# Kernel tuning notes

Hardware: AMD Instinct MI355X
Metric: run time of the kernel (lower is better)

The kernel has to match this reference:

```python
import jax, jax.numpy as jnp
import numpy as np

L, H, P = 16384, 512, 512
DT_MIN, DT_MAX = 1e-3, 1e-1


def setup_inputs() -> dict:
    key = jax.random.key(0)
    ks = jax.random.split(key, 9)
    u = jax.random.normal(ks[0], (L, H), dtype=jnp.float32)
    # stable diagonal state matrix: Re(Lambda) < 0 (HiPPO-style init)
    Lambda_re = -(0.5 * jax.random.uniform(ks[1], (P,), dtype=jnp.float32) + 1e-3)
    Lambda_im = jnp.pi * jax.random.normal(ks[2], (P,), dtype=jnp.float32)
    # lecun-normal-ish scaling for B (fan-in H) and C (fan-in P)
    B_re = jax.random.normal(ks[3], (P, H), dtype=jnp.float32) / jnp.sqrt(2.0 * H)
    B_im = jax.random.normal(ks[4], (P, H), dtype=jnp.float32) / jnp.sqrt(2.0 * H)
    C_re = jax.random.normal(ks[5], (H, P), dtype=jnp.float32) / jnp.sqrt(2.0 * P)
    C_im = jax.random.normal(ks[6], (H, P), dtype=jnp.float32) / jnp.sqrt(2.0 * P)
    D = jax.random.uniform(ks[7], (H,), dtype=jnp.float32)
    # init_log_steps: uniform in [log(dt_min), log(dt_max)]
    lo, hi = np.log(DT_MIN), np.log(DT_MAX)
    log_step = jax.random.uniform(ks[8], (P,), dtype=jnp.float32, minval=lo, maxval=hi)
    return {"u": u, "Lambda_re": Lambda_re, "Lambda_im": Lambda_im,
            "B_re": B_re, "B_im": B_im, "C_re": C_re, "C_im": C_im,
            "D": D, "log_step": log_step}


def _binary_op(q_i, q_j):
    # associative combine for diagonal linear recurrence (elementwise over (L, P))
    A_i, b_i = q_i
    A_j, b_j = q_j
    return (A_j * A_i, A_j * b_i + b_j)


def reference(u, Lambda_re, Lambda_im, B_re, B_im, C_re, C_im, D, log_step):
    Lambda = Lambda_re + 1j * Lambda_im            # (P,) complex64
    B_tilde = B_re + 1j * B_im                     # (P, H)
    C_tilde = C_re + 1j * C_im                     # (H, P)
    step = jnp.exp(log_step)                       # (P,)
    # zero-order-hold discretization
    Lambda_bar = jnp.exp(Lambda * step)            # (P,)
    B_bar = ((Lambda_bar - 1.0) / Lambda)[:, None] * B_tilde  # (P, H)
    # Bu_t = B_bar @ u_t for all t, as one GEMM: (L, H) @ (H, P)
    Bu = u.astype(B_bar.dtype) @ B_bar.T           # (L, P) complex
    Lambda_el = jnp.broadcast_to(Lambda_bar, Bu.shape)  # (L, P)
    _, xs = jax.lax.associative_scan(_binary_op, (Lambda_el, Bu))  # xs: (L, P)
    # y_t = Re(C_tilde @ x_t) + D * u_t, batched as one GEMM
    ys = (xs @ C_tilde.T).real + D * u             # (L, H)
    return ys.astype(jnp.float32)
```

## Files before the change

kernel.cpp:

```cpp
#include <hip/hip_runtime.h>
#include <stdint.h>

#define L_DIM 16384
#define H_DIM 512
#define P_DIM 512
#define T_CH  32
#define NC    (L_DIM / T_CH)
#define LP    ((size_t)L_DIM * P_DIM)
#define LH    ((size_t)L_DIM * H_DIM)

typedef unsigned short u16;
typedef __attribute__((ext_vector_type(8))) _Float16 f16x8;
typedef __attribute__((ext_vector_type(4))) float f32x4;
typedef __attribute__((ext_vector_type(8))) unsigned short u16x8;

__device__ __forceinline__ u16 f2h(float x) {
    _Float16 h = (_Float16)x;
    return __builtin_bit_cast(u16, h);
}
__device__ __forceinline__ float h2f(u16 h) {
    return (float)__builtin_bit_cast(_Float16, h);
}

__device__ __forceinline__ void gload16(const void* g, void* lds) {
    __builtin_amdgcn_global_load_lds(
        (const __attribute__((address_space(1))) void*)g,
        (__attribute__((address_space(3))) void*)(uintptr_t)lds,
        16, 0, 0);
}

__device__ __forceinline__ f32x4 mfma_f16(f16x8 a, f16x8 b, f32x4 c) {
    return __builtin_amdgcn_mfma_f32_16x16x32_f16(a, b, c, 0, 0, 0);
}

__device__ __forceinline__ void zoh_lambda(
    const float* Lre, const float* Lim, const float* log_step, int p,
    float& lr, float& li)
{
    float st = expf(log_step[p]);
    float ar = Lre[p] * st, ai = Lim[p] * st;
    float er = expf(ar);
    lr = er * cosf(ai);
    li = er * sinf(ai);
}

__global__ __launch_bounds__(256) void front_kernel(
    const float* __restrict__ u,
    const float* __restrict__ Lre, const float* __restrict__ Lim,
    const float* __restrict__ log_step,
    const float* __restrict__ Bre, const float* __restrict__ Bim,
    const float* __restrict__ Cre, const float* __restrict__ Cim,
    u16* __restrict__ uh, u16* __restrict__ Bcat, u16* __restrict__ Ccat,
    float* __restrict__ lbr, float* __restrict__ lbi,
    float* __restrict__ powr, float* __restrict__ powi)
{
    int b = blockIdx.x;
    if (b < 4096) {
        size_t i = ((size_t)b * 256 + threadIdx.x) * 8;
        float4 v0 = *(const float4*)(u + i);
        float4 v1 = *(const float4*)(u + i + 4);
        u16x8 h;
        h[0] = f2h(v0.x); h[1] = f2h(v0.y); h[2] = f2h(v0.z); h[3] = f2h(v0.w);
        h[4] = f2h(v1.x); h[5] = f2h(v1.y); h[6] = f2h(v1.z); h[7] = f2h(v1.w);
        *(u16x8*)(uh + i) = h;
    } else if (b < 5120) {
        int idx = (b - 4096) * 256 + threadIdx.x;
        int p = idx >> 9, h = idx & 511;
        float lr, li;
        zoh_lambda(Lre, Lim, log_step, p, lr, li);
        float den = Lre[p] * Lre[p] + Lim[p] * Lim[p];
        float x = lr - 1.0f, y = li;
        float gr = (x * Lre[p] + y * Lim[p]) / den;
        float gi = (y * Lre[p] - x * Lim[p]) / den;
        float br = Bre[idx], bi = Bim[idx];
        Bcat[(size_t)p * 512 + h]         = f2h(gr * br - gi * bi);
        Bcat[(size_t)(512 + p) * 512 + h] = f2h(gr * bi + gi * br);
    } else if (b < 6144) {
        int idx = (b - 5120) * 256 + threadIdx.x;
        int h = idx >> 9, p = idx & 511;
        size_t row = (size_t)h * 1024;
        Ccat[row + p]       = f2h(Cre[idx]);
        Ccat[row + 512 + p] = f2h(-Cim[idx]);
    } else {
        #pragma unroll
        for (int t = 0; t < 2; ++t) {
            int p = threadIdx.x + t * 256;
            float lr, li;
            zoh_lambda(Lre, Lim, log_step, p, lr, li);
            lbr[p] = lr; lbi[p] = li;
            float pr = 1.f, pi2 = 0.f;
            powr[p] = 1.f; powi[p] = 0.f;
            for (int k = 1; k <= T_CH; ++k) {
                float nr = pr * lr - pi2 * li;
                float ni = pr * li + pi2 * lr;
                pr = nr; pi2 = ni;
                powr[(size_t)k * P_DIM + p] = pr;
                powi[(size_t)k * P_DIM + p] = pi2;
            }
        }
    }
}

template<int KTOT, int NBN, int MODE>
__global__ __launch_bounds__(256, 2) void gemm_mfma(
    const u16* __restrict__ A0, const u16* __restrict__ A1,
    const u16* __restrict__ Bmat,
    void* __restrict__ O0v, void* __restrict__ O1v,
    const float* __restrict__ Dvec, const u16* __restrict__ uIn,
    const float* __restrict__ powr, const float* __restrict__ powi,
    float* __restrict__ Rwr, float* __restrict__ Rwi,
    float* __restrict__ Iwr, float* __restrict__ Iwi)
{
    __shared__ u16 Als[128 * 64];
    __shared__ u16 Bls[128 * 64];

    const u16* Aseg[2] = {A0, A1};

    int b = blockIdx.x;
    int m = (b & 7) * 16 + b / (8 * NBN);
    int n = (b >> 3) & (NBN - 1);
    int m0 = m * 128, n0 = n * 128;

    int tid = threadIdx.x;
    int w = tid >> 6, lane = tid & 63;
    int wm = w >> 1, wn = w & 1;

    f32x4 acc[4][4];
    #pragma unroll
    for (int i = 0; i < 4; ++i)
        #pragma unroll
        for (int j = 0; j < 4; ++j) acc[i][j] = (f32x4)0.f;

    int lr8  = lane >> 3;
    int slin = lane & 7;

    char* AlsB = (char*)&Als[0];
    char* BlsB = (char*)&Bls[0];

    const int NSEG = KTOT / 512;
    #pragma unroll
    for (int seg = 0; seg < NSEG; ++seg) {
        const u16* Ap = Aseg[seg];
        for (int k8 = 0; k8 < 8; ++k8) {
            int ko = k8 * 64;
            int kB = seg * 512 + ko;

            __syncthreads();
            #pragma unroll
            for (int c = 0; c < 4; ++c) {
                int sidx = w * 4 + c;
                int r = sidx * 8 + lr8;
                int g = slin ^ (r & 7);
                const u16* ga = Ap + (size_t)(m0 + r) * 512 + ko + g * 8;
                gload16(ga, AlsB + sidx * 1024);
                const u16* gb = Bmat + (size_t)(n0 + r) * KTOT + kB + g * 8;
                gload16(gb, BlsB + sidx * 1024);
            }
            asm volatile("s_waitcnt vmcnt(0)" ::: "memory");
            __syncthreads();

            f16x8 a[4][2], bf[4][2];
            #pragma unroll
            for (int mm = 0; mm < 4; ++mm)
                #pragma unroll
                for (int kk = 0; kk < 2; ++kk) {
                    int row = wm * 64 + mm * 16 + (lane & 15);
                    int sl  = kk * 4 + (lane >> 4);
                    int off = row * 128 + ((sl ^ (lane & 7)) << 4);
                    a[mm][kk] = *(const f16x8*)(AlsB + off);
                }
            #pragma unroll
            for (int nn = 0; nn < 4; ++nn)
                #pragma unroll
                for (int kk = 0; kk < 2; ++kk) {
                    int row = wn * 64 + nn * 16 + (lane & 15);
                    int sl  = kk * 4 + (lane >> 4);
                    int off = row * 128 + ((sl ^ (lane & 7)) << 4);
                    bf[nn][kk] = *(const f16x8*)(BlsB + off);
                }
            #pragma unroll
            for (int mm = 0; mm < 4; ++mm)
                #pragma unroll
                for (int nn = 0; nn < 4; ++nn) {
                    acc[mm][nn] = mfma_f16(a[mm][0], bf[nn][0], acc[mm][nn]);
                    acc[mm][nn] = mfma_f16(a[mm][1], bf[nn][1], acc[mm][nn]);
                }
        }
    }

    int colb = n0 + wn * 64;
    int rowb = m0 + wm * 64;
    #pragma unroll
    for (int mm = 0; mm < 4; ++mm)
        #pragma unroll
        for (int nn = 0; nn < 4; ++nn) {
            f32x4 v = acc[mm][nn];
            int col = colb + nn * 16 + (lane & 15);
            #pragma unroll
            for (int j = 0; j < 4; ++j) {
                int row = rowb + mm * 16 + (lane >> 4) * 4 + j;
                if constexpr (MODE == 0) {
                    size_t oidx = (size_t)row * 512 + (col & 511);
                    u16 hv = f2h(v[j]);
                    if (col < 512) ((u16*)O0v)[oidx] = hv;
                    else           ((u16*)O1v)[oidx] = hv;
                } else {
                    size_t oidx = (size_t)row * 512 + col;
                    ((float*)O0v)[oidx] = v[j] + Dvec[col] * h2f(uIn[oidx]);
                }
            }
        }

    if constexpr (MODE == 0) {
        float swr[2][4] = {{0.f}};
        float swi[2][4] = {{0.f}};
        #pragma unroll
        for (int h = 0; h < 2; ++h)
            #pragma unroll
            for (int j = 0; j < 4; ++j) {
                int k = h * 16 + (lane >> 4) * 4 + j;
                int e = (T_CH - 1) - k;
                #pragma unroll
                for (int nn = 0; nn < 4; ++nn) {
                    int p = (colb + nn * 16 + (lane & 15)) & 511;
                    float wr = powr[(size_t)e * 512 + p];
                    float wi = powi[(size_t)e * 512 + p];
                    swr[0][nn] = fmaf(wr, acc[h][nn][j],     swr[0][nn]);
                    swi[0][nn] = fmaf(wi, acc[h][nn][j],     swi[0][nn]);
                    swr[1][nn] = fmaf(wr, acc[2 + h][nn][j], swr[1][nn]);
                    swi[1][nn] = fmaf(wi, acc[2 + h][nn][j], swi[1][nn]);
                }
            }
        #pragma unroll
        for (int ch = 0; ch < 2; ++ch)
            #pragma unroll
            for (int nn = 0; nn < 4; ++nn) {
                float a2 = swr[ch][nn];
                a2 += __shfl_xor(a2, 16); a2 += __shfl_xor(a2, 32);
                swr[ch][nn] = a2;
                float b2 = swi[ch][nn];
                b2 += __shfl_xor(b2, 16); b2 += __shfl_xor(b2, 32);
                swi[ch][nn] = b2;
            }
        if (lane < 16) {
            #pragma unroll
            for (int ch = 0; ch < 2; ++ch) {
                int c = (m0 >> 5) + wm * 2 + ch;
                #pragma unroll
                for (int nn = 0; nn < 4; ++nn) {
                    int col = colb + nn * 16 + lane;
                    int p = col & 511;
                    size_t pidx = (size_t)c * 512 + p;
                    if (col < 512) { Rwr[pidx] = swr[ch][nn]; Rwi[pidx] = swi[ch][nn]; }
                    else           { Iwr[pidx] = swr[ch][nn]; Iwi[pidx] = swi[ch][nn]; }
                }
            }
        }
    }
}

__global__ __launch_bounds__(64) void scan_chunks(
    const float* __restrict__ Rwr, const float* __restrict__ Rwi,
    const float* __restrict__ Iwr, const float* __restrict__ Iwi,
    const float* __restrict__ powr, const float* __restrict__ powi,
    float* __restrict__ carr, float* __restrict__ cari)
{
    int p = blockIdx.x * 64 + threadIdx.x;
    float ar = powr[(size_t)T_CH * P_DIM + p];
    float ai = powi[(size_t)T_CH * P_DIM + p];
    float sr = 0.f, si = 0.f;
    #pragma unroll 8
    for (int c = 0; c < NC; ++c) {
        size_t idx = (size_t)c * P_DIM + p;
        carr[idx] = sr; cari[idx] = si;
        float vre = Rwr[idx] - Iwi[idx];
        float vim = Rwi[idx] + Iwr[idx];
        float nr = fmaf(ar, sr, fmaf(-ai, si, vre));
        float ni = fmaf(ar, si, fmaf( ai, sr, vim));
        sr = nr; si = ni;
    }
}

__global__ __launch_bounds__(P_DIM) void scan_fix(
    const u16* __restrict__ burh, const u16* __restrict__ buih,
    const float* __restrict__ lbr, const float* __restrict__ lbi,
    const float* __restrict__ carr, const float* __restrict__ cari,
    u16* __restrict__ xrh, u16* __restrict__ xih)
{
    int p = threadIdx.x;
    int c = blockIdx.x;
    float lr = lbr[p], li = lbi[p];
    float xr = carr[(size_t)c * P_DIM + p];
    float xi = cari[(size_t)c * P_DIM + p];
    size_t base = (size_t)c * T_CH * P_DIM + p;
    #pragma unroll 4
    for (int k = 0; k < T_CH; ++k) {
        size_t idx = base + (size_t)k * P_DIM;
        float br = h2f(burh[idx]), bi = h2f(buih[idx]);
        float nr = fmaf(lr, xr, fmaf(-li, xi, br));
        float ni = fmaf(lr, xi, fmaf( li, xr, bi));
        xr = nr; xi = ni;
        xrh[idx] = f2h(xr);
        xih[idx] = f2h(xi);
    }
}

extern "C" void kernel_launch(void* const* d_in, const int* in_sizes, int n_in,
                              void* d_out, int out_size, void* d_ws, size_t ws_size,
                              hipStream_t stream)
{
    const float* u        = (const float*)d_in[0];
    const float* Lre      = (const float*)d_in[1];
    const float* Lim      = (const float*)d_in[2];
    const float* Bre      = (const float*)d_in[3];
    const float* Bim      = (const float*)d_in[4];
    const float* Cre      = (const float*)d_in[5];
    const float* Cim      = (const float*)d_in[6];
    const float* D        = (const float*)d_in[7];
    const float* log_step = (const float*)d_in[8];
    float* out = (float*)d_out;

    char* w8 = (char*)d_ws;
    u16*   burh = (u16*)(w8);
    u16*   buih = (u16*)(w8 + 16777216);
    u16*   xrh  = (u16*)(w8 + 33554432);
    u16*   xih  = (u16*)(w8 + 50331648);
    u16*   uh   = (u16*)(w8 + 67108864);
    u16*   Bcat = (u16*)(w8 + 83886080);
    u16*   Ccat = (u16*)(w8 + 84934656);
    float* Rwr  = (float*)(w8 + 85983232);
    float* Rwi  = (float*)(w8 + 87031808);
    float* Iwr  = (float*)(w8 + 88080384);
    float* Iwi  = (float*)(w8 + 89128960);
    float* carr = (float*)(w8 + 90177536);
    float* cari = (float*)(w8 + 91226112);
    float* powr = (float*)(w8 + 92274688);
    float* powi = (float*)(w8 + 92342272);
    float* lbr  = (float*)(w8 + 92409856);
    float* lbi  = lbr + P_DIM;

    front_kernel<<<6145, 256, 0, stream>>>(
        u, Lre, Lim, log_step, Bre, Bim, Cre, Cim,
        uh, Bcat, Ccat, lbr, lbi, powr, powi);

    gemm_mfma<512, 8, 0><<<1024, 256, 0, stream>>>(
        uh, uh, Bcat, burh, buih, nullptr, nullptr,
        powr, powi, Rwr, Rwi, Iwr, Iwi);

    scan_chunks<<<8, 64, 0, stream>>>(Rwr, Rwi, Iwr, Iwi, powr, powi, carr, cari);
    scan_fix<<<NC, P_DIM, 0, stream>>>(burh, buih, lbr, lbi, carr, cari, xrh, xih);

    gemm_mfma<1024, 4, 1><<<512, 256, 0, stream>>>(
        xrh, xih, Ccat, out, nullptr, D, uh,
        nullptr, nullptr, nullptr, nullptr, nullptr, nullptr);
}
```

Baseline: 121.9 us.

## Fuse intra-chunk scan fixup into output GEMM, computing x tiles in LDS

Removes the scan_fix kernel and its fp16 xr/xi intermediate buffers. The output GEMM now rebuilds each 64-column slice of the state tile in LDS by running the 32-step recurrence from the chunk carries, then multiplies it against both the real and imaginary halves of C. This cuts a launch and a full (L,P) complex write plus re-read through global memory. The cost is a serial recurrence inside the GEMM main loop, done per k-slice by a single wave per chunk, along with doubled LDS usage that may lower occupancy. The burh/buih loads are strided by 512 elements across k.

```diff
diff --git a/kernel.cpp b/kernel.cpp
--- a/kernel.cpp
+++ b/kernel.cpp
@@ -101,20 +101,17 @@
     }
 }
 
-template<int KTOT, int NBN, int MODE>
-__global__ __launch_bounds__(256, 2) void gemm_mfma(
-    const u16* __restrict__ A0, const u16* __restrict__ A1,
+__global__ __launch_bounds__(256, 2) void gemm_bu(
+    const u16* __restrict__ A0,
     const u16* __restrict__ Bmat,
-    void* __restrict__ O0v, void* __restrict__ O1v,
-    const float* __restrict__ Dvec, const u16* __restrict__ uIn,
+    u16* __restrict__ O0, u16* __restrict__ O1,
     const float* __restrict__ powr, const float* __restrict__ powi,
     float* __restrict__ Rwr, float* __restrict__ Rwi,
     float* __restrict__ Iwr, float* __restrict__ Iwi)
 {
+    const int NBN = 8;
     __shared__ u16 Als[128 * 64];
     __shared__ u16 Bls[128 * 64];
-
-    const u16* Aseg[2] = {A0, A1};
 
     int b = blockIdx.x;
     int m = (b & 7) * 16 + b / (8 * NBN);
@@ -137,55 +134,47 @@
     char* AlsB = (char*)&Als[0];
     char* BlsB = (char*)&Bls[0];
 
-    const int NSEG = KTOT / 512;
-    #pragma unroll
-    for (int seg = 0; seg < NSEG; ++seg) {
-        const u16* Ap = Aseg[seg];
-        for (int k8 = 0; k8 < 8; ++k8) {
-            int ko = k8 * 64;
-            int kB = seg * 512 + ko;
-
-            __syncthreads();
-            #pragma unroll
-            for (int c = 0; c < 4; ++c) {
-                int sidx = w * 4 + c;
-                int r = sidx * 8 + lr8;
-                int g = slin ^ (r & 7);
-                const u16* ga = Ap + (size_t)(m0 + r) * 512 + ko + g * 8;
-                gload16(ga, AlsB + sidx * 1024);
-                const u16* gb = Bmat + (size_t)(n0 + r) * KTOT + kB + g * 8;
-                gload16(gb, BlsB + sidx * 1024);
-            }
-            asm volatile("s_waitcnt vmcnt(0)" ::: "memory");
-            __syncthreads();
-
-            f16x8 a[4][2], bf[4][2];
-            #pragma unroll
-            for (int mm = 0; mm < 4; ++mm)
-                #pragma unroll
-                for (int kk = 0; kk < 2; ++kk) {
-                    int row = wm * 64 + mm * 16 + (lane & 15);
-                    int sl  = kk * 4 + (lane >> 4);
-                    int off = row * 128 + ((sl ^ (lane & 7)) << 4);
-                    a[mm][kk] = *(const f16x8*)(AlsB + off);
-                }
-            #pragma unroll
-            for (int nn = 0; nn < 4; ++nn)
-                #pragma unroll
-                for (int kk = 0; kk < 2; ++kk) {
-                    int row = wn * 64 + nn * 16 + (lane & 15);
-                    int sl  = kk * 4 + (lane >> 4);
-                    int off = row * 128 + ((sl ^ (lane & 7)) << 4);
-                    bf[nn][kk] = *(const f16x8*)(BlsB + off);
-                }
-            #pragma unroll
-            for (int mm = 0; mm < 4; ++mm)
-                #pragma unroll
-                for (int nn = 0; nn < 4; ++nn) {
-                    acc[mm][nn] = mfma_f16(a[mm][0], bf[nn][0], acc[mm][nn]);
-                    acc[mm][nn] = mfma_f16(a[mm][1], bf[nn][1], acc[mm][nn]);
-                }
-        }
+    for (int k8 = 0; k8 < 8; ++k8) {
+        int ko = k8 * 64;
+
+        __syncthreads();
+        #pragma unroll
+        for (int c = 0; c < 4; ++c) {
+            int sidx = w * 4 + c;
+            int r = sidx * 8 + lr8;
+            int g = slin ^ (r & 7);
+            gload16(A0   + (size_t)(m0 + r) * 512 + ko + g * 8, AlsB + sidx * 1024);
+            gload16(Bmat + (size_t)(n0 + r) * 512 + ko + g * 8, BlsB + sidx * 1024);
+        }
+        asm volatile("s_waitcnt vmcnt(0)" ::: "memory");
+        __syncthreads();
+
+        f16x8 a[4][2], bf[4][2];
+        #pragma unroll
+        for (int mm = 0; mm < 4; ++mm)
+            #pragma unroll
+            for (int kk = 0; kk < 2; ++kk) {
+                int row = wm * 64 + mm * 16 + (lane & 15);
+                int sl  = kk * 4 + (lane >> 4);
+                int off = row * 128 + ((sl ^ (lane & 7)) << 4);
+                a[mm][kk] = *(const f16x8*)(AlsB + off);
+            }
+        #pragma unroll
+        for (int nn = 0; nn < 4; ++nn)
+            #pragma unroll
+            for (int kk = 0; kk < 2; ++kk) {
+                int row = wn * 64 + nn * 16 + (lane & 15);
+                int sl  = kk * 4 + (lane >> 4);
+                int off = row * 128 + ((sl ^ (lane & 7)) << 4);
+                bf[nn][kk] = *(const f16x8*)(BlsB + off);
+            }
+        #pragma unroll
+        for (int mm = 0; mm < 4; ++mm)
+            #pragma unroll
+            for (int nn = 0; nn < 4; ++nn) {
+                acc[mm][nn] = mfma_f16(a[mm][0], bf[nn][0], acc[mm][nn]);
+                acc[mm][nn] = mfma_f16(a[mm][1], bf[nn][1], acc[mm][nn]);
+            }
     }
 
     int colb = n0 + wn * 64;
@@ -199,61 +188,54 @@
             #pragma unroll
             for (int j = 0; j < 4; ++j) {
                 int row = rowb + mm * 16 + (lane >> 4) * 4 + j;
-                if constexpr (MODE == 0) {
-                    size_t oidx = (size_t)row * 512 + (col & 511);
-                    u16 hv = f2h(v[j]);
-                    if (col < 512) ((u16*)O0v)[oidx] = hv;
-                    else           ((u16*)O1v)[oidx] = hv;
-                } else {
-                    size_t oidx = (size_t)row * 512 + col;
-                    ((float*)O0v)[oidx] = v[j] + Dvec[col] * h2f(uIn[oidx]);
-                }
-            }
-        }
-
-    if constexpr (MODE == 0) {
-        float swr[2][4] = {{0.f}};
-        float swi[2][4] = {{0.f}};
-        #pragma unroll
-        for (int h = 0; h < 2; ++h)
-            #pragma unroll
-            for (int j = 0; j < 4; ++j) {
-                int k = h * 16 + (lane >> 4) * 4 + j;
-                int e = (T_CH - 1) - k;
-                #pragma unroll
-                for (int nn = 0; nn < 4; ++nn) {
-                    int p = (colb + nn * 16 + (lane & 15)) & 511;
-                    float wr = powr[(size_t)e * 512 + p];
-                    float wi = powi[(size_t)e * 512 + p];
-                    swr[0][nn] = fmaf(wr, acc[h][nn][j],     swr[0][nn]);
-                    swi[0][nn] = fmaf(wi, acc[h][nn][j],     swi[0][nn]);
-                    swr[1][nn] = fmaf(wr, acc[2 + h][nn][j], swr[1][nn]);
-                    swi[1][nn] = fmaf(wi, acc[2 + h][nn][j], swi[1][nn]);
-                }
-            }
-        #pragma unroll
-        for (int ch = 0; ch < 2; ++ch)
+                size_t oidx = (size_t)row * 512 + (col & 511);
+                u16 hv = f2h(v[j]);
+                if (col < 512) O0[oidx] = hv;
+                else           O1[oidx] = hv;
+            }
+        }
+
+    float swr[2][4] = {{0.f}};
+    float swi[2][4] = {{0.f}};
+    #pragma unroll
+    for (int h = 0; h < 2; ++h)
+        #pragma unroll
+        for (int j = 0; j < 4; ++j) {
+            int k = h * 16 + (lane >> 4) * 4 + j;
+            int e = (T_CH - 1) - k;
             #pragma unroll
             for (int nn = 0; nn < 4; ++nn) {
-                float a2 = swr[ch][nn];
-                a2 += __shfl_xor(a2, 16); a2 += __shfl_xor(a2, 32);
-                swr[ch][nn] = a2;
-                float b2 = swi[ch][nn];
-                b2 += __shfl_xor(b2, 16); b2 += __shfl_xor(b2, 32);
-                swi[ch][nn] = b2;
-            }
-        if (lane < 16) {
-            #pragma unroll
-            for (int ch = 0; ch < 2; ++ch) {
-                int c = (m0 >> 5) + wm * 2 + ch;
-                #pragma unroll
-                for (int nn = 0; nn < 4; ++nn) {
-                    int col = colb + nn * 16 + lane;
-                    int p = col & 511;
-                    size_t pidx = (size_t)c * 512 + p;
-                    if (col < 512) { Rwr[pidx] = swr[ch][nn]; Rwi[pidx] = swi[ch][nn]; }
-                    else           { Iwr[pidx] = swr[ch][nn]; Iwi[pidx] = swi[ch][nn]; }
-                }
+                int p = (colb + nn * 16 + (lane & 15)) & 511;
+                float wr = powr[(size_t)e * 512 + p];
+                float wi = powi[(size_t)e * 512 + p];
+                swr[0][nn] = fmaf(wr, acc[h][nn][j],     swr[0][nn]);
+                swi[0][nn] = fmaf(wi, acc[h][nn][j],     swi[0][nn]);
+                swr[1][nn] = fmaf(wr, acc[2 + h][nn][j], swr[1][nn]);
+                swi[1][nn] = fmaf(wi, acc[2 + h][nn][j], swi[1][nn]);
+            }
+        }
+    #pragma unroll
+    for (int ch = 0; ch < 2; ++ch)
+        #pragma unroll
+        for (int nn = 0; nn < 4; ++nn) {
+            float a2 = swr[ch][nn];
+            a2 += __shfl_xor(a2, 16); a2 += __shfl_xor(a2, 32);
+            swr[ch][nn] = a2;
+            float b2 = swi[ch][nn];
+            b2 += __shfl_xor(b2, 16); b2 += __shfl_xor(b2, 32);
+            swi[ch][nn] = b2;
+        }
+    if (lane < 16) {
+        #pragma unroll
+        for (int ch = 0; ch < 2; ++ch) {
+            int c = (m0 >> 5) + wm * 2 + ch;
+            #pragma unroll
+            for (int nn = 0; nn < 4; ++nn) {
+                int col = colb + nn * 16 + lane;
+                int p = col & 511;
+                size_t pidx = (size_t)c * 512 + p;
+                if (col < 512) { Rwr[pidx] = swr[ch][nn]; Rwi[pidx] = swi[ch][nn]; }
+                else           { Iwr[pidx] = swr[ch][nn]; Iwi[pidx] = swi[ch][nn]; }
             }
         }
     }
@@ -281,28 +263,157 @@
     }
 }
 
-__global__ __launch_bounds__(P_DIM) void scan_fix(
+__global__ __launch_bounds__(256, 2) void gemm_y_fused(
     const u16* __restrict__ burh, const u16* __restrict__ buih,
+    const u16* __restrict__ Ccat,
     const float* __restrict__ lbr, const float* __restrict__ lbi,
     const float* __restrict__ carr, const float* __restrict__ cari,
-    u16* __restrict__ xrh, u16* __restrict__ xih)
-{
-    int p = threadIdx.x;
-    int c = blockIdx.x;
-    float lr = lbr[p], li = lbi[p];
-    float xr = carr[(size_t)c * P_DIM + p];
-    float xi = cari[(size_t)c * P_DIM + p];
-    size_t base = (size_t)c * T_CH * P_DIM + p;
-    #pragma unroll 4
-    for (int k = 0; k < T_CH; ++k) {
-        size_t idx = base + (size_t)k * P_DIM;
-        float br = h2f(burh[idx]), bi = h2f(buih[idx]);
-        float nr = fmaf(lr, xr, fmaf(-li, xi, br));
-        float ni = fmaf(lr, xi, fmaf( li, xr, bi));
-        xr = nr; xi = ni;
-        xrh[idx] = f2h(xr);
-        xih[idx] = f2h(xi);
+    const float* __restrict__ Dvec, const u16* __restrict__ uIn,
+    float* __restrict__ out)
+{
+    __shared__ u16 Axr[128 * 64];
+    __shared__ u16 Axi[128 * 64];
+    __shared__ u16 Bl0[128 * 64];
+    __shared__ u16 Bl1[128 * 64];
+
+    int b = blockIdx.x;
+    int m = (b & 7) * 16 + b / 32;
+    int n = (b >> 3) & 3;
+    int m0 = m * 128, n0 = n * 128;
+
+    int tid = threadIdx.x;
+    int w = tid >> 6, lane = tid & 63;
+    int wm = w >> 1, wn = w & 1;
+
+    f32x4 acc[4][4];
+    #pragma unroll
+    for (int i = 0; i < 4; ++i)
+        #pragma unroll
+        for (int j = 0; j < 4; ++j) acc[i][j] = (f32x4)0.f;
+
+    int lr8  = lane >> 3;
+    int slin = lane & 7;
+
+    char* AxrB = (char*)&Axr[0];
+    char* AxiB = (char*)&Axi[0];
+    char* B0B  = (char*)&Bl0[0];
+    char* B1B  = (char*)&Bl1[0];
+
+    int ch = w;
+    int cglob = m * 4 + ch;
+
+    for (int q = 0; q < 8; ++q) {
+        int kB0 = q * 64;
+        int kB1 = 512 + q * 64;
+
+        __syncthreads();
+        #pragma unroll
+        for (int c = 0; c < 4; ++c) {
+            int sidx = w * 4 + c;
+            int r = sidx * 8 + lr8;
+            int g = slin ^ (r & 7);
+            gload16(Ccat + (size_t)(n0 + r) * 1024 + kB0 + g * 8, B0B + sidx * 1024);
+            gload16(Ccat + (size_t)(n0 + r) * 1024 + kB1 + g * 8, B1B + sidx * 1024);
+        }
+
+        {
+            int p = q * 64 + lane;
+            float lr_ = lbr[p], li_ = lbi[p];
+            float xr = carr[(size_t)cglob * 512 + p];
+            float xi = cari[(size_t)cglob * 512 + p];
+            size_t gbase = (size_t)(m0 + ch * 32) * 512 + p;
+            int rloc = ch * 32;
+            int gsel = lane >> 3;
+            int boff = (lane & 7) * 2;
+            #pragma unroll 4
+            for (int k = 0; k < 32; ++k) {
+                float br = h2f(burh[gbase + (size_t)k * 512]);
+                float bi = h2f(buih[gbase + (size_t)k * 512]);
+                float nr = fmaf(lr_, xr, fmaf(-li_, xi, br));
+                float ni = fmaf(lr_, xi, fmaf( li_, xr, bi));
+                xr = nr; xi = ni;
+                int r = rloc + k;
+                int off = r * 128 + ((gsel ^ (r & 7)) << 4) + boff;
+                *(u16*)(AxrB + off) = f2h(nr);
+                *(u16*)(AxiB + off) = f2h(ni);
+            }
+        }
+        asm volatile("s_waitcnt vmcnt(0)" ::: "memory");
+        __syncthreads();
+
+        {
+            f16x8 a[4][2], bf[4][2];
+            #pragma unroll
+            for (int mm = 0; mm < 4; ++mm)
+                #pragma unroll
+                for (int kk = 0; kk < 2; ++kk) {
+                    int row = wm * 64 + mm * 16 + (lane & 15);
+                    int sl  = kk * 4 + (lane >> 4);
+                    int off = row * 128 + ((sl ^ (lane & 7)) << 4);
+                    a[mm][kk] = *(const f16x8*)(AxrB + off);
+                }
+            #pragma unroll
+            for (int nn = 0; nn < 4; ++nn)
+                #pragma unroll
+                for (int kk = 0; kk < 2; ++kk) {
+                    int row = wn * 64 + nn * 16 + (lane & 15);
+                    int sl  = kk * 4 + (lane >> 4);
+                    int off = row * 128 + ((sl ^ (lane & 7)) << 4);
+                    bf[nn][kk] = *(const f16x8*)(B0B + off);
+                }
+            #pragma unroll
+            for (int mm = 0; mm < 4; ++mm)
+                #pragma unroll
+                for (int nn = 0; nn < 4; ++nn) {
+                    acc[mm][nn] = mfma_f16(a[mm][0], bf[nn][0], acc[mm][nn]);
+                    acc[mm][nn] = mfma_f16(a[mm][1], bf[nn][1], acc[mm][nn]);
+                }
+        }
+        {
+            f16x8 a[4][2], bf[4][2];
+            #pragma unroll
+            for (int mm = 0; mm < 4; ++mm)
+                #pragma unroll
+                for (int kk = 0; kk < 2; ++kk) {
+                    int row = wm * 64 + mm * 16 + (lane & 15);
+                    int sl  = kk * 4 + (lane >> 4);
+                    int off = row * 128 + ((sl ^ (lane & 7)) << 4);
+                    a[mm][kk] = *(const f16x8*)(AxiB + off);
+                }
+            #pragma unroll
+            for (int nn = 0; nn < 4; ++nn)
+                #pragma unroll
+                for (int kk = 0; kk < 2; ++kk) {
+                    int row = wn * 64 + nn * 16 + (lane & 15);
+                    int sl  = kk * 4 + (lane >> 4);
+                    int off = row * 128 + ((sl ^ (lane & 7)) << 4);
+                    bf[nn][kk] = *(const f16x8*)(B1B + off);
+                }
+            #pragma unroll
+            for (int mm = 0; mm < 4; ++mm)
+                #pragma unroll
+                for (int nn = 0; nn < 4; ++nn) {
+                    acc[mm][nn] = mfma_f16(a[mm][0], bf[nn][0], acc[mm][nn]);
+                    acc[mm][nn] = mfma_f16(a[mm][1], bf[nn][1], acc[mm][nn]);
+                }
+        }
     }
+
+    int colb = n0 + wn * 64;
+    int rowb = m0 + wm * 64;
+    #pragma unroll
+    for (int mm = 0; mm < 4; ++mm)
+        #pragma unroll
+        for (int nn = 0; nn < 4; ++nn) {
+            f32x4 v = acc[mm][nn];
+            int col = colb + nn * 16 + (lane & 15);
+            #pragma unroll
+            for (int j = 0; j < 4; ++j) {
+                int row = rowb + mm * 16 + (lane >> 4) * 4 + j;
+                size_t oidx = (size_t)row * 512 + col;
+                out[oidx] = v[j] + Dvec[col] * h2f(uIn[oidx]);
+            }
+        }
 }
 
 extern "C" void kernel_launch(void* const* d_in, const int* in_sizes, int n_in,
@@ -323,34 +434,29 @@
     char* w8 = (char*)d_ws;
     u16*   burh = (u16*)(w8);
     u16*   buih = (u16*)(w8 + 16777216);
-    u16*   xrh  = (u16*)(w8 + 33554432);
-    u16*   xih  = (u16*)(w8 + 50331648);
-    u16*   uh   = (u16*)(w8 + 67108864);
-    u16*   Bcat = (u16*)(w8 + 83886080);
-    u16*   Ccat = (u16*)(w8 + 84934656);
-    float* Rwr  = (float*)(w8 + 85983232);
-    float* Rwi  = (float*)(w8 + 87031808);
-    float* Iwr  = (float*)(w8 + 88080384);
-    float* Iwi  = (float*)(w8 + 89128960);
-    float* carr = (float*)(w8 + 90177536);
-    float* cari = (float*)(w8 + 91226112);
-    float* powr = (float*)(w8 + 92274688);
-    float* powi = (float*)(w8 + 92342272);
-    float* lbr  = (float*)(w8 + 92409856);
+    u16*   uh   = (u16*)(w8 + 33554432);
+    u16*   Bcat = (u16*)(w8 + 50331648);
+    u16*   Ccat = (u16*)(w8 + 51380224);
+    float* Rwr  = (float*)(w8 + 52428800);
+    float* Rwi  = (float*)(w8 + 53477376);
+    float* Iwr  = (float*)(w8 + 54525952);
+    float* Iwi  = (float*)(w8 + 55574528);
+    float* carr = (float*)(w8 + 56623104);
+    float* cari = (float*)(w8 + 57671680);
+    float* powr = (float*)(w8 + 58720256);
+    float* powi = (float*)(w8 + 58787840);
+    float* lbr  = (float*)(w8 + 58855424);
     float* lbi  = lbr + P_DIM;
 
     front_kernel<<<6145, 256, 0, stream>>>(
         u, Lre, Lim, log_step, Bre, Bim, Cre, Cim,
         uh, Bcat, Ccat, lbr, lbi, powr, powi);
 
-    gemm_mfma<512, 8, 0><<<1024, 256, 0, stream>>>(
-        uh, uh, Bcat, burh, buih, nullptr, nullptr,
-        powr, powi, Rwr, Rwi, Iwr, Iwi);
+    gemm_bu<<<1024, 256, 0, stream>>>(
+        uh, Bcat, burh, buih, powr, powi, Rwr, Rwi, Iwr, Iwi);
 
     scan_chunks<<<8, 64, 0, stream>>>(Rwr, Rwi, Iwr, Iwi, powr, powi, carr, cari);
-    scan_fix<<<NC, P_DIM, 0, stream>>>(burh, buih, lbr, lbi, carr, cari, xrh, xih);
-
-    gemm_mfma<1024, 4, 1><<<512, 256, 0, stream>>>(
-        xrh, xih, Ccat, out, nullptr, D, uh,
-        nullptr, nullptr, nullptr, nullptr, nullptr, nullptr);
-}
+
+    gemm_y_fused<<<512, 256, 0, stream>>>(
+        burh, buih, Ccat, lbr, lbi, carr, cari, D, uh, out);
+}
```

Result: slower. 125.5 us (median of 2 runs) (+2.9%).
